# Performance work log

Hardware: AMD Instinct MI355X
Metric: run time of the kernel (lower is better)

The kernel has to match this reference:

```python
import jax, jax.numpy as jnp
import numpy as np

# Model dims: E experts, T total routed tokens, D model dim, H expert hidden dim
E, T, D, H = 8, 16384, 2048, 5632


def setup_inputs() -> dict:
    key = jax.random.key(0)
    k1, k2, k3, k4 = jax.random.split(key, 4)
    init_std = 0.02
    x = jax.random.normal(k1, (T, D), dtype=jnp.float32)
    # w1/w3: (num_experts, hidden_dim, dim); w2: (num_experts, dim, hidden_dim)
    w1 = jax.random.normal(k2, (E, H, D), dtype=jnp.float32) * init_std
    w2 = jax.random.normal(k3, (E, D, H), dtype=jnp.float32) * init_std
    w3 = jax.random.normal(k4, (E, H, D), dtype=jnp.float32) * init_std
    # Tokens are pre-sorted by expert; even split so sum == T (no padding path)
    num_tokens_per_expert = jnp.full((E,), T // E, dtype=jnp.int32)
    return {"x": x, "w1": w1, "w2": w2, "w3": w3,
            "num_tokens_per_expert": num_tokens_per_expert}


def reference(x, w1, w2, w3, num_tokens_per_expert):
    """Grouped-GEMM SwiGLU experts: out[t] = silu(x@w1[e].T) * (x@w3[e].T) @ w2[e].T
    where e is the expert owning token t (tokens sorted by expert).
    lax.ragged_dot is the exact grouped-GEMM primitive: lhs (m,k), rhs (g,k,n),
    group_sizes (g,) -> (m,n). Weights are stored as (g, out, in), so swap to (g, in, out),
    matching the torch matmul with transpose(-2, -1).
    """
    groups = num_tokens_per_expert.astype(jnp.int32)
    gate = jax.lax.ragged_dot(x, jnp.swapaxes(w1, 1, 2), groups)   # (T, H)
    up = jax.lax.ragged_dot(x, jnp.swapaxes(w3, 1, 2), groups)     # (T, H)
    h = jax.nn.silu(gate) * up                                      # fused SwiGLU
    out = jax.lax.ragged_dot(h, jnp.swapaxes(w2, 1, 2), groups)    # (T, D)
    return out
```

## Files before the change

### kernel.cpp

```cpp
#include <hip/hip_runtime.h>
#include <hip/hip_bf16.h>


typedef __bf16 bf16x8 __attribute__((ext_vector_type(8)));
typedef float f32x4 __attribute__((ext_vector_type(4)));
typedef unsigned short u16x8 __attribute__((ext_vector_type(8)));

constexpr int E = 8;
constexpr int T = 16384;
constexpr int D = 2048;
constexpr int H = 5632;

#define DEV static __device__ __forceinline__

DEV unsigned short f2bf(float f) {
    unsigned u = __builtin_bit_cast(unsigned, f);
    u = (u + 0x7FFFu + ((u >> 16) & 1u)) >> 16;
    return (unsigned short)u;
}

DEV void gload16(const void* g, void* l) {
    __builtin_amdgcn_global_load_lds(
        (const __attribute__((address_space(1))) void*)g,
        (__attribute__((address_space(3))) void*)l, 16, 0, 0);
}

DEV f32x4 mfma16(bf16x8 a, bf16x8 b, f32x4 c) {
    return __builtin_amdgcn_mfma_f32_16x16x32_bf16(a, b, c, 0, 0, 0);
}

DEV void cvt8(const float* src, unsigned short* dst) {
    float4 a = *(const float4*)src;
    float4 c = *(const float4*)(src + 4);
    u16x8 r;
    r[0] = f2bf(a.x); r[1] = f2bf(a.y); r[2] = f2bf(a.z); r[3] = f2bf(a.w);
    r[4] = f2bf(c.x); r[5] = f2bf(c.y); r[6] = f2bf(c.z); r[7] = f2bf(c.w);
    *(u16x8*)dst = r;
}

__global__ __launch_bounds__(256) void k_cvt_pre(
    const float* __restrict__ x, const float* __restrict__ w1,
    const float* __restrict__ w3, unsigned short* __restrict__ xb,
    unsigned short* __restrict__ w13b) {
    const int bid = blockIdx.x, tid = threadIdx.x;
    if (bid < 512) {
        const long n8 = (long)T * D / 8;
        for (long i = (long)bid * 256 + tid; i < n8; i += 512L * 256)
            cvt8(x + i * 8, xb + i * 8);
    } else {
        const int which = (bid < 1280) ? 0 : 1;
        const float* src = which ? w3 : w1;
        const long b0 = which ? 1280 : 512;
        const long n8 = (long)E * H * D / 8;
        for (long i = ((long)bid - b0) * 256 + tid; i < n8; i += 768L * 256) {
            int col8 = (int)(i & 255);
            int rowi = (int)(i >> 8);
            int e = rowi / H;
            int h = rowi - e * H;
            int rr = ((h >> 4) << 5) + (which << 4) + (h & 15);
            cvt8(src + i * 8,
                 w13b + ((size_t)e * (2 * H) + rr) * D + (size_t)col8 * 8);
        }
    }
}

__global__ __launch_bounds__(256) void k_cvt(const float* __restrict__ in,
                                             unsigned short* __restrict__ out,
                                             long n8) {
    long i = (long)blockIdx.x * blockDim.x + threadIdx.x;
    long stride = (long)gridDim.x * blockDim.x;
    for (; i < n8; i += stride) cvt8(in + i * 8, out + i * 8);
}

DEV int expert_of_row(const int* __restrict__ ntp, int row0) {
    int e = 0, s = 0;
    for (int i = 0; i < E; ++i) {
        int c = ntp[i];
        if (row0 < s + c) { e = i; break; }
        s += c;
    }
    return e;
}

template <int LD, int NT>
DEV void gemm_4p(const unsigned short* pa, const unsigned short* pb,
                 unsigned short* sA, unsigned short* sB, int tid,
                 f32x4 (&acc)[8][4]) {
    const int lane = tid & 63, wid = tid >> 6;
    const int wm = wid >> 2, wn = wid & 3;

    const int q8 = (((lane >> 4) ^ ((lane >> 1) & 3)) << 3);
    const int aoff = (wm * 128 + (lane & 15)) * 32 + q8;
    const int boff = (wn * 64 + (lane & 15)) * 32 + q8;

    char* lA = (char*)sA;
    char* lB = (char*)sB;
    const int dW = wid << 10;

    auto stA = [&](int t, int kk) {
        const unsigned short* g = pa + (size_t)t * 64 + kk * 32;
        char* l = lA + ((t & 1) << 15) + (kk << 14) + dW;
        gload16(g, l);
        gload16(g + (size_t)128 * LD, l + 8192);
    };
    auto stB = [&](int t, int kk) {
        const unsigned short* g = pb + (size_t)t * 64 + kk * 32;
        char* l = lB + ((t & 1) << 15) + (kk << 14) + dW;
        gload16(g, l);
        gload16(g + (size_t)128 * LD, l + 8192);
    };

    stA(0, 0); stB(0, 0); stA(0, 1); stB(0, 1);
    asm volatile("s_waitcnt vmcnt(4)" ::: "memory");
    __builtin_amdgcn_s_barrier();

#pragma unroll 1
    for (int t = 0; t < NT; ++t) {
        const int sb = (t & 1) << 14;
        const unsigned short* A0 = sA + sb + aoff;
        const unsigned short* B0 = sB + sb + boff;
        const unsigned short* A1 = A0 + 8192;
        const unsigned short* B1 = B0 + 8192;
        const bool more = (t + 1 < NT);
        bf16x8 a[4], b[4];

#pragma unroll
        for (int i = 0; i < 4; ++i) a[i] = *(const bf16x8*)(A0 + i * 512);
#pragma unroll
        for (int i = 0; i < 4; ++i) b[i] = *(const bf16x8*)(B0 + i * 512);
        if (more) stA(t + 1, 0);
        __builtin_amdgcn_s_barrier();
        asm volatile("s_waitcnt lgkmcnt(0)" ::: "memory");
        __builtin_amdgcn_sched_barrier(0);
        __builtin_amdgcn_s_setprio(1);
#pragma unroll
        for (int m = 0; m < 4; ++m)
#pragma unroll
            for (int n = 0; n < 4; ++n)
                acc[m][n] = mfma16(a[m], b[n], acc[m][n]);
        __builtin_amdgcn_s_setprio(0);
        __builtin_amdgcn_s_barrier();

#pragma unroll
        for (int i = 0; i < 4; ++i)
            a[i] = *(const bf16x8*)(A0 + 2048 + i * 512);
        if (more) {
            stB(t + 1, 0);
            asm volatile("s_waitcnt vmcnt(4)" ::: "memory");
        } else {
            asm volatile("s_waitcnt vmcnt(0)" ::: "memory");
        }
        __builtin_amdgcn_s_barrier();
        asm volatile("s_waitcnt lgkmcnt(0)" ::: "memory");
        __builtin_amdgcn_sched_barrier(0);
        __builtin_amdgcn_s_setprio(1);
#pragma unroll
        for (int m = 0; m < 4; ++m)
#pragma unroll
            for (int n = 0; n < 4; ++n)
                acc[4 + m][n] = mfma16(a[m], b[n], acc[4 + m][n]);
        __builtin_amdgcn_s_setprio(0);
        __builtin_amdgcn_s_barrier();

#pragma unroll
        for (int i = 0; i < 4; ++i) a[i] = *(const bf16x8*)(A1 + i * 512);
#pragma unroll
        for (int i = 0; i < 4; ++i) b[i] = *(const bf16x8*)(B1 + i * 512);
        if (more) stA(t + 1, 1);
        __builtin_amdgcn_s_barrier();
        asm volatile("s_waitcnt lgkmcnt(0)" ::: "memory");
        __builtin_amdgcn_sched_barrier(0);
        __builtin_amdgcn_s_setprio(1);
#pragma unroll
        for (int m = 0; m < 4; ++m)
#pragma unroll
            for (int n = 0; n < 4; ++n)
                acc[m][n] = mfma16(a[m], b[n], acc[m][n]);
        __builtin_amdgcn_s_setprio(0);
        __builtin_amdgcn_s_barrier();

#pragma unroll
        for (int i = 0; i < 4; ++i)
            a[i] = *(const bf16x8*)(A1 + 2048 + i * 512);
        if (more) {
            stB(t + 1, 1);
            asm volatile("s_waitcnt vmcnt(4)" ::: "memory");
        }
        __builtin_amdgcn_s_barrier();
        asm volatile("s_waitcnt lgkmcnt(0)" ::: "memory");
        __builtin_amdgcn_sched_barrier(0);
        __builtin_amdgcn_s_setprio(1);
#pragma unroll
        for (int m = 0; m < 4; ++m)
#pragma unroll
            for (int n = 0; n < 4; ++n)
                acc[4 + m][n] = mfma16(a[m], b[n], acc[4 + m][n]);
        __builtin_amdgcn_s_setprio(0);
        __builtin_amdgcn_s_barrier();
    }
}

__global__ __launch_bounds__(512, 2) void k_gate_up(
    const unsigned short* __restrict__ xb,
    const unsigned short* __restrict__ w13b,
    const float* __restrict__ w2, unsigned short* __restrict__ w2b,
    const int* __restrict__ ntp, unsigned short* __restrict__ hbuf) {
    __shared__ unsigned short sA[2 * 2 * 8192];
    __shared__ unsigned short sB[2 * 2 * 8192];

    const int bid = blockIdx.x;
    const int tid = threadIdx.x;

    if (w2) {
        const float* src = w2 + (size_t)bid * 32768;
        unsigned short* dst = w2b + (size_t)bid * 32768;
#pragma unroll
        for (int it = 0; it < 8; ++it) {
            int o = (it * 512 + tid) * 8;
            cvt8(src + o, dst + o);
        }
        asm volatile("s_waitcnt vmcnt(0)" ::: "memory");
    }

    const int tm = (bid & 7) * 8 + ((bid >> 3) & 7);
    const int tn = bid >> 6;

    const int row0 = tm << 8;
    const int e = expert_of_row(ntp, row0);
    const int lane = tid & 63, wid = tid >> 6;

    const int sr = tid >> 2;
    const int sq = (tid & 3) ^ ((tid >> 3) & 3);
    const unsigned short* pa = xb + (size_t)(row0 + sr) * D + sq * 8;
    const unsigned short* pb = w13b + (size_t)e * (2 * H) * D +
                               (size_t)((tn << 8) + sr) * D + sq * 8;

    f32x4 acc[8][4] = {};
    gemm_4p<D, D / 64>(pa, pb, sA, sB, tid, acc);

    const int wm = wid >> 2, wn = wid & 3;
    const int rbase = row0 + (wm << 7) + ((lane >> 4) << 2);
    const int cb = (((tn << 3) + (wn << 1)) << 4) + (lane & 15);
#pragma unroll
    for (int mi = 0; mi < 8; ++mi)
#pragma unroll
        for (int pi = 0; pi < 2; ++pi) {
            f32x4 g = acc[mi][2 * pi], u = acc[mi][2 * pi + 1];
            const int hcol = cb + (pi << 4);
#pragma unroll
            for (int j = 0; j < 4; ++j) {
                float gv = g[j];
                float hv = gv * u[j] / (1.f + __expf(-gv));
                hbuf[(size_t)(rbase + (mi << 4) + j) * H + hcol] = f2bf(hv);
            }
        }
}

__global__ __launch_bounds__(512, 2) void k_down(
    const unsigned short* __restrict__ hbuf,
    const unsigned short* __restrict__ w2b,
    const int* __restrict__ ntp,
    float* __restrict__ out) {
    __shared__ unsigned short sA[2 * 2 * 8192];
    __shared__ unsigned short sB[2 * 2 * 8192];

    const int nwg = gridDim.x;
    const int cpx = nwg >> 3;
    const int bid = blockIdx.x;
    const int swz = (bid & 7) * cpx + (bid >> 3);
    const int tm = swz & 63;
    const int tn = swz >> 6;

    const int row0 = tm << 8;
    const int e = expert_of_row(ntp, row0);
    const int tid = threadIdx.x;
    const int lane = tid & 63, wid = tid >> 6;

    const int sr = tid >> 2;
    const int sq = (tid & 3) ^ ((tid >> 3) & 3);
    const unsigned short* pa = hbuf + (size_t)(row0 + sr) * H + sq * 8;
    const unsigned short* pb = w2b + (size_t)e * D * H +
                               (size_t)((tn << 8) + sr) * H + sq * 8;

    f32x4 acc[8][4] = {};
    gemm_4p<H, H / 64>(pa, pb, sA, sB, tid, acc);

    const int wm = wid >> 2, wn = wid & 3;
    const int rbase = row0 + (wm << 7) + ((lane >> 4) << 2);
    const int cb = (tn << 8) + (wn << 6) + (lane & 15);
#pragma unroll
    for (int mi = 0; mi < 8; ++mi)
#pragma unroll
        for (int ni = 0; ni < 4; ++ni) {
            f32x4 c = acc[mi][ni];
#pragma unroll
            for (int j = 0; j < 4; ++j)
                out[(size_t)(rbase + (mi << 4) + j) * D + cb + (ni << 4)] =
                    c[j];
        }
}

extern "C" void kernel_launch(void* const* d_in, const int* in_sizes, int n_in,
                              void* d_out, int out_size, void* d_ws,
                              size_t ws_size, hipStream_t stream) {
    const float* x = (const float*)d_in[0];
    const float* w1 = (const float*)d_in[1];
    const float* w2 = (const float*)d_in[2];
    const float* w3 = (const float*)d_in[3];
    const int* ntp = (const int*)d_in[4];
    float* out = (float*)d_out;

    char* ws = (char*)d_ws;
    unsigned short* xb = (unsigned short*)(ws + 0);
    unsigned short* w13b = (unsigned short*)(ws + 67108864L);
    unsigned short* hbuf = (unsigned short*)(ws + 436207616L);
    const bool big = ws_size >= 805306368UL;
    unsigned short* w2b = big ? (unsigned short*)(ws + 620756992L) : w13b;

    k_cvt_pre<<<2048, 256, 0, stream>>>(x, w1, w3, xb, w13b);

    k_gate_up<<<(T / 256) * (2 * H / 256), 512, 0, stream>>>(
        xb, w13b, big ? w2 : nullptr, big ? w2b : nullptr, ntp, hbuf);

    if (!big)
        k_cvt<<<2048, 256, 0, stream>>>(w2, w2b, (long)E * D * H / 8);

    k_down<<<(T / 256) * (D / 256), 512, 0, stream>>>(hbuf, w2b, ntp, out);
}
```

Baseline: 1.416 ms.

## Switch GEMM to 256x128 tiles with 3-stage LDS ring and fewer barriers

Replaces the 256x256-tile, 8-wave double-buffered GEMM with a 256x128-tile, 4-wave kernel that has a triple-buffered LDS ring over K-steps of 32. Loads are issued two stages ahead, and there is one barrier per K-step instead of several. The grid doubles and the XCD-aware tile mapping is recomputed, which changes L2 reuse. Arithmetic intensity per block drops and the K loop gets twice as many iterations, in exchange for less barrier stalling and deeper prefetch.

After: 1.691 ms. 1.19x slower.

```diff
diff --git a/kernel.cpp b/kernel.cpp
--- a/kernel.cpp
+++ b/kernel.cpp
@@ -37,6 +37,8 @@
     r[4] = f2bf(c.x); r[5] = f2bf(c.y); r[6] = f2bf(c.z); r[7] = f2bf(c.w);
     *(u16x8*)dst = r;
 }
+
+DEV void SB() { __builtin_amdgcn_sched_barrier(0); }
 
 __global__ __launch_bounds__(256) void k_cvt_pre(
     const float* __restrict__ x, const float* __restrict__ w1,
@@ -83,55 +85,56 @@
 }
 
 template <int LD, int NT>
-DEV void gemm_4p(const unsigned short* pa, const unsigned short* pb,
+DEV void gemm_r3(const unsigned short* pa, const unsigned short* pb,
                  unsigned short* sA, unsigned short* sB, int tid,
                  f32x4 (&acc)[8][4]) {
     const int lane = tid & 63, wid = tid >> 6;
-    const int wm = wid >> 2, wn = wid & 3;
+    const int wm = wid >> 1, wn = wid & 1;
 
     const int q8 = (((lane >> 4) ^ ((lane >> 1) & 3)) << 3);
     const int aoff = (wm * 128 + (lane & 15)) * 32 + q8;
     const int boff = (wn * 64 + (lane & 15)) * 32 + q8;
 
-    char* lA = (char*)sA;
-    char* lB = (char*)sB;
-    const int dW = wid << 10;
-
-    auto stA = [&](int t, int kk) {
-        const unsigned short* g = pa + (size_t)t * 64 + kk * 32;
-        char* l = lA + ((t & 1) << 15) + (kk << 14) + dW;
-        gload16(g, l);
-        gload16(g + (size_t)128 * LD, l + 8192);
+    char* cA = (char*)sA;
+    char* cB = (char*)sB;
+    const int dA = wid << 12;
+    const int dB = wid << 11;
+
+    auto stA = [&](int t, int slot) {
+        const unsigned short* g = pa + (size_t)t * 32;
+        char* l = cA + slot * 16384 + dA;
+#pragma unroll
+        for (int i = 0; i < 4; ++i)
+            gload16(g + (size_t)i * 16 * LD, l + i * 1024);
     };
-    auto stB = [&](int t, int kk) {
-        const unsigned short* g = pb + (size_t)t * 64 + kk * 32;
-        char* l = lB + ((t & 1) << 15) + (kk << 14) + dW;
-        gload16(g, l);
-        gload16(g + (size_t)128 * LD, l + 8192);
+    auto stB = [&](int t, int slot) {
+        const unsigned short* g = pb + (size_t)t * 32;
+        char* l = cB + slot * 8192 + dB;
+#pragma unroll
+        for (int i = 0; i < 2; ++i)
+            gload16(g + (size_t)i * 16 * LD, l + i * 1024);
     };
 
-    stA(0, 0); stB(0, 0); stA(0, 1); stB(0, 1);
-    asm volatile("s_waitcnt vmcnt(4)" ::: "memory");
+    stA(0, 0); stB(0, 0);
+    stA(1, 1); stB(1, 1);
+    asm volatile("s_waitcnt vmcnt(6)" ::: "memory");
     __builtin_amdgcn_s_barrier();
 
+    int scur = 0, sstg = 2;
 #pragma unroll 1
     for (int t = 0; t < NT; ++t) {
-        const int sb = (t & 1) << 14;
-        const unsigned short* A0 = sA + sb + aoff;
-        const unsigned short* B0 = sB + sb + boff;
-        const unsigned short* A1 = A0 + 8192;
-        const unsigned short* B1 = B0 + 8192;
-        const bool more = (t + 1 < NT);
+        const unsigned short* A = sA + scur * 8192 + aoff;
+        const unsigned short* B = sB + scur * 4096 + boff;
+        const bool s2 = (t + 2 < NT);
         bf16x8 a[4], b[4];
 
 #pragma unroll
-        for (int i = 0; i < 4; ++i) a[i] = *(const bf16x8*)(A0 + i * 512);
-#pragma unroll
-        for (int i = 0; i < 4; ++i) b[i] = *(const bf16x8*)(B0 + i * 512);
-        if (more) stA(t + 1, 0);
-        __builtin_amdgcn_s_barrier();
+        for (int i = 0; i < 4; ++i) a[i] = *(const bf16x8*)(A + i * 512);
+#pragma unroll
+        for (int i = 0; i < 4; ++i) b[i] = *(const bf16x8*)(B + i * 512);
+        if (s2) stA(t + 2, sstg);
         asm volatile("s_waitcnt lgkmcnt(0)" ::: "memory");
-        __builtin_amdgcn_sched_barrier(0);
+        SB();
         __builtin_amdgcn_s_setprio(1);
 #pragma unroll
         for (int m = 0; m < 4; ++m)
@@ -139,20 +142,13 @@
             for (int n = 0; n < 4; ++n)
                 acc[m][n] = mfma16(a[m], b[n], acc[m][n]);
         __builtin_amdgcn_s_setprio(0);
-        __builtin_amdgcn_s_barrier();
 
 #pragma unroll
         for (int i = 0; i < 4; ++i)
-            a[i] = *(const bf16x8*)(A0 + 2048 + i * 512);
-        if (more) {
-            stB(t + 1, 0);
-            asm volatile("s_waitcnt vmcnt(4)" ::: "memory");
-        } else {
-            asm volatile("s_waitcnt vmcnt(0)" ::: "memory");
-        }
-        __builtin_amdgcn_s_barrier();
+            a[i] = *(const bf16x8*)(A + 2048 + i * 512);
+        if (s2) stB(t + 2, sstg);
         asm volatile("s_waitcnt lgkmcnt(0)" ::: "memory");
-        __builtin_amdgcn_sched_barrier(0);
+        SB();
         __builtin_amdgcn_s_setprio(1);
 #pragma unroll
         for (int m = 0; m < 4; ++m)
@@ -160,87 +156,61 @@
             for (int n = 0; n < 4; ++n)
                 acc[4 + m][n] = mfma16(a[m], b[n], acc[4 + m][n]);
         __builtin_amdgcn_s_setprio(0);
+
+        if (s2)               asm volatile("s_waitcnt vmcnt(6)" ::: "memory");
+        else if (t + 1 < NT)  asm volatile("s_waitcnt vmcnt(0)" ::: "memory");
         __builtin_amdgcn_s_barrier();
-
-#pragma unroll
-        for (int i = 0; i < 4; ++i) a[i] = *(const bf16x8*)(A1 + i * 512);
-#pragma unroll
-        for (int i = 0; i < 4; ++i) b[i] = *(const bf16x8*)(B1 + i * 512);
-        if (more) stA(t + 1, 1);
-        __builtin_amdgcn_s_barrier();
-        asm volatile("s_waitcnt lgkmcnt(0)" ::: "memory");
-        __builtin_amdgcn_sched_barrier(0);
-        __builtin_amdgcn_s_setprio(1);
-#pragma unroll
-        for (int m = 0; m < 4; ++m)
-#pragma unroll
-            for (int n = 0; n < 4; ++n)
-                acc[m][n] = mfma16(a[m], b[n], acc[m][n]);
-        __builtin_amdgcn_s_setprio(0);
-        __builtin_amdgcn_s_barrier();
-
-#pragma unroll
-        for (int i = 0; i < 4; ++i)
-            a[i] = *(const bf16x8*)(A1 + 2048 + i * 512);
-        if (more) {
-            stB(t + 1, 1);
-            asm volatile("s_waitcnt vmcnt(4)" ::: "memory");
-        }
-        __builtin_amdgcn_s_barrier();
-        asm volatile("s_waitcnt lgkmcnt(0)" ::: "memory");
-        __builtin_amdgcn_sched_barrier(0);
-        __builtin_amdgcn_s_setprio(1);
-#pragma unroll
-        for (int m = 0; m < 4; ++m)
-#pragma unroll
-            for (int n = 0; n < 4; ++n)
-                acc[4 + m][n] = mfma16(a[m], b[n], acc[4 + m][n]);
-        __builtin_amdgcn_s_setprio(0);
-        __builtin_amdgcn_s_barrier();
-    }
-}
-
-__global__ __launch_bounds__(512, 2) void k_gate_up(
+        SB();
+
+        sstg = scur;
+        scur = (scur == 2) ? 0 : scur + 1;
+    }
+}
+
+__global__ __launch_bounds__(256, 2) void k_gate_up(
     const unsigned short* __restrict__ xb,
     const unsigned short* __restrict__ w13b,
     const float* __restrict__ w2, unsigned short* __restrict__ w2b,
     const int* __restrict__ ntp, unsigned short* __restrict__ hbuf) {
-    __shared__ unsigned short sA[2 * 2 * 8192];
-    __shared__ unsigned short sB[2 * 2 * 8192];
+    __shared__ unsigned short sA[3 * 8192];
+    __shared__ unsigned short sB[3 * 4096];
 
     const int bid = blockIdx.x;
     const int tid = threadIdx.x;
 
     if (w2) {
-        const float* src = w2 + (size_t)bid * 32768;
-        unsigned short* dst = w2b + (size_t)bid * 32768;
+        const float* src = w2 + (size_t)bid * 16384;
+        unsigned short* dst = w2b + (size_t)bid * 16384;
 #pragma unroll
         for (int it = 0; it < 8; ++it) {
-            int o = (it * 512 + tid) * 8;
+            int o = (it * 256 + tid) * 8;
             cvt8(src + o, dst + o);
         }
         asm volatile("s_waitcnt vmcnt(0)" ::: "memory");
     }
 
-    const int tm = (bid & 7) * 8 + ((bid >> 3) & 7);
-    const int tn = bid >> 6;
+    const int xcd = bid & 7;
+    const int j = bid >> 3;
+    const int tn = j % 88;
+    const int tm = xcd * 8 + j / 88;
 
     const int row0 = tm << 8;
     const int e = expert_of_row(ntp, row0);
     const int lane = tid & 63, wid = tid >> 6;
 
-    const int sr = tid >> 2;
-    const int sq = (tid & 3) ^ ((tid >> 3) & 3);
-    const unsigned short* pa = xb + (size_t)(row0 + sr) * D + sq * 8;
+    const int sq = (lane & 3) ^ ((lane >> 3) & 3);
+    const int ar = (wid << 6) + (lane >> 2);
+    const int br = (wid << 5) + (lane >> 2);
+    const unsigned short* pa = xb + (size_t)(row0 + ar) * D + sq * 8;
     const unsigned short* pb = w13b + (size_t)e * (2 * H) * D +
-                               (size_t)((tn << 8) + sr) * D + sq * 8;
+                               (size_t)((tn << 7) + br) * D + sq * 8;
 
     f32x4 acc[8][4] = {};
-    gemm_4p<D, D / 64>(pa, pb, sA, sB, tid, acc);
-
-    const int wm = wid >> 2, wn = wid & 3;
+    gemm_r3<D, D / 32>(pa, pb, sA, sB, tid, acc);
+
+    const int wm = wid >> 1, wn = wid & 1;
     const int rbase = row0 + (wm << 7) + ((lane >> 4) << 2);
-    const int cb = (((tn << 3) + (wn << 1)) << 4) + (lane & 15);
+    const int cb = (((tn << 2) + (wn << 1)) << 4) + (lane & 15);
 #pragma unroll
     for (int mi = 0; mi < 8; ++mi)
 #pragma unroll
@@ -248,55 +218,55 @@
             f32x4 g = acc[mi][2 * pi], u = acc[mi][2 * pi + 1];
             const int hcol = cb + (pi << 4);
 #pragma unroll
-            for (int j = 0; j < 4; ++j) {
-                float gv = g[j];
-                float hv = gv * u[j] / (1.f + __expf(-gv));
-                hbuf[(size_t)(rbase + (mi << 4) + j) * H + hcol] = f2bf(hv);
+            for (int jj = 0; jj < 4; ++jj) {
+                float gv = g[jj];
+                float hv = gv * u[jj] / (1.f + __expf(-gv));
+                hbuf[(size_t)(rbase + (mi << 4) + jj) * H + hcol] = f2bf(hv);
             }
         }
 }
 
-__global__ __launch_bounds__(512, 2) void k_down(
+__global__ __launch_bounds__(256, 2) void k_down(
     const unsigned short* __restrict__ hbuf,
     const unsigned short* __restrict__ w2b,
     const int* __restrict__ ntp,
     float* __restrict__ out) {
-    __shared__ unsigned short sA[2 * 2 * 8192];
-    __shared__ unsigned short sB[2 * 2 * 8192];
-
-    const int nwg = gridDim.x;
-    const int cpx = nwg >> 3;
+    __shared__ unsigned short sA[3 * 8192];
+    __shared__ unsigned short sB[3 * 4096];
+
     const int bid = blockIdx.x;
-    const int swz = (bid & 7) * cpx + (bid >> 3);
-    const int tm = swz & 63;
-    const int tn = swz >> 6;
+    const int tid = threadIdx.x;
+    const int xcd = bid & 7;
+    const int j = bid >> 3;
+    const int tn = j & 15;
+    const int tm = xcd * 8 + (j >> 4);
 
     const int row0 = tm << 8;
     const int e = expert_of_row(ntp, row0);
-    const int tid = threadIdx.x;
     const int lane = tid & 63, wid = tid >> 6;
 
-    const int sr = tid >> 2;
-    const int sq = (tid & 3) ^ ((tid >> 3) & 3);
-    const unsigned short* pa = hbuf + (size_t)(row0 + sr) * H + sq * 8;
+    const int sq = (lane & 3) ^ ((lane >> 3) & 3);
+    const int ar = (wid << 6) + (lane >> 2);
+    const int br = (wid << 5) + (lane >> 2);
+    const unsigned short* pa = hbuf + (size_t)(row0 + ar) * H + sq * 8;
     const unsigned short* pb = w2b + (size_t)e * D * H +
-                               (size_t)((tn << 8) + sr) * H + sq * 8;
+                               (size_t)((tn << 7) + br) * H + sq * 8;
 
     f32x4 acc[8][4] = {};
-    gemm_4p<H, H / 64>(pa, pb, sA, sB, tid, acc);
-
-    const int wm = wid >> 2, wn = wid & 3;
+    gemm_r3<H, H / 32>(pa, pb, sA, sB, tid, acc);
+
+    const int wm = wid >> 1, wn = wid & 1;
     const int rbase = row0 + (wm << 7) + ((lane >> 4) << 2);
-    const int cb = (tn << 8) + (wn << 6) + (lane & 15);
+    const int cb = (tn << 7) + (wn << 6) + (lane & 15);
 #pragma unroll
     for (int mi = 0; mi < 8; ++mi)
 #pragma unroll
         for (int ni = 0; ni < 4; ++ni) {
             f32x4 c = acc[mi][ni];
 #pragma unroll
-            for (int j = 0; j < 4; ++j)
-                out[(size_t)(rbase + (mi << 4) + j) * D + cb + (ni << 4)] =
-                    c[j];
+            for (int jj = 0; jj < 4; ++jj)
+                out[(size_t)(rbase + (mi << 4) + jj) * D + cb + (ni << 4)] =
+                    c[jj];
         }
 }
 
@@ -319,11 +289,11 @@
 
     k_cvt_pre<<<2048, 256, 0, stream>>>(x, w1, w3, xb, w13b);
 
-    k_gate_up<<<(T / 256) * (2 * H / 256), 512, 0, stream>>>(
+    k_gate_up<<<(T / 256) * (2 * H / 128), 256, 0, stream>>>(
         xb, w13b, big ? w2 : nullptr, big ? w2b : nullptr, ntp, hbuf);
 
     if (!big)
         k_cvt<<<2048, 256, 0, stream>>>(w2, w2b, (long)E * D * H / 8);
 
-    k_down<<<(T / 256) * (D / 256), 512, 0, stream>>>(hbuf, w2b, ntp, out);
-}
+    k_down<<<(T / 256) * (D / 128), 256, 0, stream>>>(hbuf, w2b, ntp, out);
+}
```
